# Kernel tuning notes

Measured on AMD Instinct MI355X. Metric: run time of the kernel, lower is better.

## Reference

```python
import jax, jax.numpy as jnp
import numpy as np

N = 50000      # number of genes
E = 1_600_000  # number of GRP edges
F = 256        # feature dim


def setup_inputs() -> dict:
    key = jax.random.key(0)
    k1, k2, k3 = jax.random.split(key, 3)
    indices = jax.random.randint(k1, (2, E), 0, N, dtype=jnp.int64 if jax.config.jax_enable_x64 else jnp.int32)
    values = jax.random.normal(k2, (E,), dtype=jnp.float32)
    mat_2 = jax.random.normal(k3, (N, F), dtype=jnp.float32)
    return {"indices": indices, "values": values, "n": N, "mat_2": mat_2}


def reference(indices, values, n, mat_2):
    # Sparse COO [n, n] @ dense [n, F]:
    # out[r] = sum over edges e with row[e]==r of values[e] * mat_2[col[e]]
    row, col = indices[0], indices[1]
    msgs = values[:, None] * mat_2[col]            # [E, F] gathered messages
    out = jax.ops.segment_sum(msgs, row, num_segments=n)  # [n, F]
    return out
```

## Files before the change

### kernel.cpp

```cpp
#include <hip/hip_runtime.h>

#define F_DIM   256
#define OVFCAP  8192
#define MAXBUCK 1024
#define BCAP    2560
#define P1_TILE 8192
#define WINB    13
#define MAXPASS 8
#define RCAP2   16
#define ELLK    64

struct OvfEdge { int r, c; float v; };

__device__ __forceinline__ unsigned short f32_to_bf16(float x) {
    unsigned u = __float_as_uint(x);
    unsigned r = (u + 0x7FFFu + ((u >> 16) & 1u)) >> 16;
    return (unsigned short)r;
}

__device__ __forceinline__ void gfma(unsigned e, int lane,
                                     const unsigned short* __restrict__ mb, float4& acc) {
    int   col = (int)(e >> 16);
    float v   = __uint_as_float((e & 0xFFFFu) << 16);
    ushort4 m = ((const ushort4*)(mb + ((long long)col << 8)))[lane];
    acc.x += v * __uint_as_float((unsigned)m.x << 16);
    acc.y += v * __uint_as_float((unsigned)m.y << 16);
    acc.z += v * __uint_as_float((unsigned)m.z << 16);
    acc.w += v * __uint_as_float((unsigned)m.w << 16);
}

__global__ void cvt_kernel(const float* __restrict__ src,
                           unsigned short* __restrict__ dst, int n4) {
    int t = blockIdx.x * blockDim.x + threadIdx.x;
    if (t >= n4) return;
    float4 f = ((const float4*)src)[t];
    ushort4 o;
    o.x = f32_to_bf16(f.x); o.y = f32_to_bf16(f.y);
    o.z = f32_to_bf16(f.z); o.w = f32_to_bf16(f.w);
    ((ushort4*)dst)[t] = o;
}

__global__ void __launch_bounds__(1024)
build_kernel(const int* __restrict__ rows, const int* __restrict__ cols,
             const float* __restrict__ vals,
             const float* __restrict__ mat2, unsigned short* __restrict__ mb, int n4,
             int* __restrict__ gcur, int2* __restrict__ ebuf,
             int* __restrict__ ovfcnt, OvfEdge* __restrict__ ovf,
             int E, int nbuck, int p1blocks) {
    __shared__ int s_cnt[MAXBUCK];
    __shared__ int s_base[MAXBUCK];
    __shared__ int s_cur[MAXBUCK];
    const int t = threadIdx.x;
    const int bid = blockIdx.x;

    if (bid >= p1blocks) {
        int i = (bid - p1blocks) * 1024 + t;
        if (i < n4) {
            float4 f = ((const float4*)mat2)[i];
            ushort4 o;
            o.x = f32_to_bf16(f.x); o.y = f32_to_bf16(f.y);
            o.z = f32_to_bf16(f.z); o.w = f32_to_bf16(f.w);
            ((ushort4*)mb)[i] = o;
        }
        return;
    }

    for (int i = t; i < nbuck; i += 1024) { s_cnt[i] = 0; s_cur[i] = 0; }
    __syncthreads();

    const long long e0 = (long long)bid * P1_TILE;
    int4 r4[2], c4[2]; float4 v4[2];
    #pragma unroll
    for (int k = 0; k < 2; ++k) {
        long long i = e0 + (long long)k * 4096 + (long long)t * 4;
        if (i + 3 < E) {
            r4[k] = *(const int4*)(rows + i);
            c4[k] = *(const int4*)(cols + i);
            v4[k] = *(const float4*)(vals + i);
        } else {
            r4[k] = make_int4(-1, -1, -1, -1);
            c4[k] = make_int4(0, 0, 0, 0);
            v4[k] = make_float4(0.f, 0.f, 0.f, 0.f);
            #pragma unroll
            for (int j = 0; j < 4; ++j) {
                long long ii = i + j;
                if (ii < E) {
                    (&r4[k].x)[j] = rows[ii];
                    (&c4[k].x)[j] = cols[ii];
                    (&v4[k].x)[j] = vals[ii];
                }
            }
        }
        #pragma unroll
        for (int j = 0; j < 4; ++j) {
            int rr = (&r4[k].x)[j];
            if (rr >= 0) atomicAdd(&s_cnt[rr >> 6], 1);
        }
    }
    __syncthreads();
    for (int i = t; i < nbuck; i += 1024) {
        int c_ = s_cnt[i];
        s_base[i] = c_ ? atomicAdd(&gcur[i], c_) : 0;
    }
    __syncthreads();
    #pragma unroll
    for (int k = 0; k < 2; ++k) {
        #pragma unroll
        for (int j = 0; j < 4; ++j) {
            int rr = (&r4[k].x)[j];
            if (rr < 0) continue;
            int cc = (&c4[k].x)[j];
            float vv = (&v4[k].x)[j];
            int b = rr >> 6;
            int sl = s_base[b] + atomicAdd(&s_cur[b], 1);
            if (sl < BCAP) {
                ebuf[(long long)b * BCAP + sl] =
                    make_int2((int)(((unsigned)cc << 16) | f32_to_bf16(vv)), rr & 63);
            } else {
                int o = atomicAdd(ovfcnt, 1);
                if (o < OVFCAP) { ovf[o].r = rr; ovf[o].c = cc; ovf[o].v = vv; }
            }
        }
    }
}

__global__ void __launch_bounds__(512, 6)
spmm_pass_kernel(const int* __restrict__ gcur, const int2* __restrict__ ebuf,
                 const unsigned short* __restrict__ mb,
                 float* __restrict__ out, int N,
                 int* __restrict__ ovfcnt, OvfEdge* __restrict__ ovf) {
    __shared__ int2 sorted[BCAP];
    __shared__ unsigned ell_s[2][64 * RCAP2];
    __shared__ int cur_s[2][64];
    __shared__ int pcnt[8][MAXPASS];
    __shared__ int pcur[8][MAXPASS];
    __shared__ int soff[64];

    const int t = threadIdx.x, b = blockIdx.x;
    const int wid = t >> 6, lane = t & 63;
    const int hw = t >> 5, fl = t & 31;
    const int npass = (N + (1 << WINB) - 1) >> WINB;
    const int cnt = min(gcur[b], BCAP);
    const int2* eb = ebuf + (long long)b * BCAP;

    if (t < 8 * MAXPASS) { ((int*)pcnt)[t] = 0; ((int*)pcur)[t] = 0; }
    if (t < 128) ((int*)cur_s)[t] = 0;
    #pragma unroll
    for (int q = 0; q < (2 * 64 * RCAP2) / 512; ++q) ((unsigned*)ell_s)[t + q * 512] = 0u;
    __syncthreads();

    int2 e4[5]; int pid[5]; int nv = 0;
    #pragma unroll
    for (int k = 0; k < 5; ++k) {
        int j = t + k * 512;
        if (j < cnt) {
            e4[nv] = eb[j];
            pid[nv] = (int)((unsigned)e4[nv].x >> (16 + WINB));
            atomicAdd(&pcnt[wid][pid[nv]], 1);
            ++nv;
        }
    }
    __syncthreads();

    if (wid == 0) {
        int val = pcnt[lane & 7][lane >> 3];
        int x = val;
        #pragma unroll
        for (int off = 1; off < 64; off <<= 1) {
            int y = __shfl_up(x, off);
            if (lane >= off) x += y;
        }
        soff[lane] = x - val;
    }
    __syncthreads();

    for (int k = 0; k < nv; ++k) {
        int p = pid[k];
        int pos = atomicAdd(&pcur[wid][p], 1);
        sorted[soff[p * 8 + wid] + pos] = e4[k];
    }
    __syncthreads();

    {
        int beg = soff[0];
        int end = (npass > 1) ? soff[8] : cnt;
        for (int j = beg + t; j < end; j += 512) {
            int2 e = sorted[j];
            int pos = atomicAdd(&cur_s[0][e.y], 1);
            if (pos < RCAP2) ell_s[0][(e.y << 4) | pos] = (unsigned)e.x;
            else {
                int o = atomicAdd(ovfcnt, 1);
                if (o < OVFCAP) {
                    ovf[o].r = b * 64 + e.y;
                    ovf[o].c = (int)((unsigned)e.x >> 16);
                    ovf[o].v = __uint_as_float(((unsigned)e.x & 0xFFFFu) << 16);
                }
            }
        }
    }
    __syncthreads();

    float acc[4][8];
    #pragma unroll
    for (int r = 0; r < 4; ++r)
        #pragma unroll
        for (int q = 0; q < 8; ++q) acc[r][q] = 0.f;

    for (int p = 0; p < npass; ++p) {
        const int cur = p & 1, nxt = cur ^ 1;

        if (p + 1 < npass) {
            int beg = soff[(p + 1) * 8];
            int end = (p + 2 < npass) ? soff[(p + 2) * 8] : cnt;
            for (int j = beg + t; j < end; j += 512) {
                int2 e = sorted[j];
                int pos = atomicAdd(&cur_s[nxt][e.y], 1);
                if (pos < RCAP2) ell_s[nxt][(e.y << 4) | pos] = (unsigned)e.x;
                else {
                    int o = atomicAdd(ovfcnt, 1);
                    if (o < OVFCAP) {
                        ovf[o].r = b * 64 + e.y;
                        ovf[o].c = (int)((unsigned)e.x >> 16);
                        ovf[o].v = __uint_as_float(((unsigned)e.x & 0xFFFFu) << 16);
                    }
                }
            }
        }

        #pragma unroll
        for (int ri = 0; ri < 4; ++ri) {
            const int rr = hw + (ri << 4);
            int deg = min(cur_s[cur][rr], RCAP2);
            int padded = (deg + 3) & ~3;
            for (int j = 0; j < padded; j += 4) {
                int4 m[4]; float v[4];
                #pragma unroll
                for (int k = 0; k < 4; ++k) {
                    unsigned e = ell_s[cur][(rr << 4) + j + k];
                    v[k] = __uint_as_float((e & 0xFFFFu) << 16);
                    m[k] = ((const int4*)(mb + ((long long)(e >> 16) << 8)))[fl];
                }
                #pragma unroll
                for (int k = 0; k < 4; ++k) {
                    acc[ri][0] += v[k] * __uint_as_float((unsigned)m[k].x << 16);
                    acc[ri][1] += v[k] * __uint_as_float((unsigned)m[k].x & 0xFFFF0000u);
                    acc[ri][2] += v[k] * __uint_as_float((unsigned)m[k].y << 16);
                    acc[ri][3] += v[k] * __uint_as_float((unsigned)m[k].y & 0xFFFF0000u);
                    acc[ri][4] += v[k] * __uint_as_float((unsigned)m[k].z << 16);
                    acc[ri][5] += v[k] * __uint_as_float((unsigned)m[k].z & 0xFFFF0000u);
                    acc[ri][6] += v[k] * __uint_as_float((unsigned)m[k].w << 16);
                    acc[ri][7] += v[k] * __uint_as_float((unsigned)m[k].w & 0xFFFF0000u);
                }
            }
            #pragma unroll
            for (int z = fl; z < RCAP2; z += 32) ell_s[cur][(rr << 4) + z] = 0u;
            if (fl == 0) cur_s[cur][rr] = 0;
        }
        __syncthreads();
    }

    #pragma unroll
    for (int ri = 0; ri < 4; ++ri) {
        const int rr = hw + (ri << 4);
        long long gr = (long long)b * 64 + rr;
        if (gr < N) {
            float4* op = (float4*)(out + (gr << 8) + (fl << 3));
            op[0] = make_float4(acc[ri][0], acc[ri][1], acc[ri][2], acc[ri][3]);
            op[1] = make_float4(acc[ri][4], acc[ri][5], acc[ri][6], acc[ri][7]);
        }
    }
}

__global__ void ovf_kernel(const int* __restrict__ ovfcnt,
                           const OvfEdge* __restrict__ ovf,
                           const float* __restrict__ mat2,
                           float* __restrict__ out) {
    int cnt = min(*ovfcnt, OVFCAP);
    int lane = threadIdx.x & 63;
    int wid = threadIdx.x >> 6;
    for (int e = wid; e < cnt; e += 4) {
        OvfEdge ed = ovf[e];
        float4 m = ((const float4*)(mat2 + (long long)ed.c * F_DIM))[lane];
        float* dst = out + (long long)ed.r * F_DIM + lane * 4;
        unsafeAtomicAdd(dst + 0, ed.v * m.x);
        unsafeAtomicAdd(dst + 1, ed.v * m.y);
        unsafeAtomicAdd(dst + 2, ed.v * m.z);
        unsafeAtomicAdd(dst + 3, ed.v * m.w);
    }
}

__device__ __forceinline__ void scatter_one(int r, int c, float v,
                                            int* cursor, unsigned* ell,
                                            int* ovfcnt, OvfEdge* ovf) {
    int pos = atomicAdd(&cursor[r], 1);
    if (pos < ELLK) {
        ell[(long long)r * ELLK + pos] = ((unsigned)c << 16) | f32_to_bf16(v);
    } else {
        int o = atomicAdd(ovfcnt, 1);
        if (o < OVFCAP) { ovf[o].r = r; ovf[o].c = c; ovf[o].v = v; }
    }
}

__global__ void scatter_ell_kernel(const int* __restrict__ rows,
                                   const int* __restrict__ cols,
                                   const float* __restrict__ vals,
                                   int* __restrict__ cursor,
                                   unsigned* __restrict__ ell,
                                   int* __restrict__ ovfcnt,
                                   OvfEdge* __restrict__ ovf, int E) {
    int t = blockIdx.x * blockDim.x + threadIdx.x;
    int i0 = t * 4;
    if (i0 + 3 < E) {
        int4   r = *(const int4*)(rows + i0);
        int4   c = *(const int4*)(cols + i0);
        float4 v = *(const float4*)(vals + i0);
        scatter_one(r.x, c.x, v.x, cursor, ell, ovfcnt, ovf);
        scatter_one(r.y, c.y, v.y, cursor, ell, ovfcnt, ovf);
        scatter_one(r.z, c.z, v.z, cursor, ell, ovfcnt, ovf);
        scatter_one(r.w, c.w, v.w, cursor, ell, ovfcnt, ovf);
    } else {
        for (int i = i0; i < E; ++i)
            scatter_one(rows[i], cols[i], vals[i], cursor, ell, ovfcnt, ovf);
    }
}

template <bool BF16MAT>
__global__ void __launch_bounds__(256)
spmm_ell_kernel(const int* __restrict__ cursor,
                const unsigned* __restrict__ ell,
                const unsigned short* __restrict__ mb,
                const float* __restrict__ mat2,
                float* __restrict__ out, int N) {
    int wave = (int)(((long long)blockIdx.x * blockDim.x + threadIdx.x) >> 6);
    int lane = threadIdx.x & 63;
    if (wave >= N) return;
    int deg = min(cursor[wave], ELLK);
    unsigned pk = (lane < deg) ? ell[(long long)wave * ELLK + lane] : 0u;
    float4 acc = make_float4(0.f, 0.f, 0.f, 0.f);
    int padded = (deg + 7) & ~7;
    for (int j = 0; j < padded; j += 8) {
        #pragma unroll
        for (int k = 0; k < 8; ++k) {
            unsigned e = (unsigned)__shfl((int)pk, j + k);
            if (BF16MAT) {
                gfma(e, lane, mb, acc);
            } else {
                int   col = (int)(e >> 16);
                float v   = __uint_as_float((e & 0xFFFFu) << 16);
                float4 m = ((const float4*)(mat2 + ((long long)col << 8)))[lane];
                acc.x += v * m.x; acc.y += v * m.y;
                acc.z += v * m.z; acc.w += v * m.w;
            }
        }
    }
    ((float4*)(out + ((long long)wave << 8)))[lane] = acc;
}

__global__ void spmm_atomic_kernel(const int* __restrict__ rows,
                                   const int* __restrict__ cols,
                                   const float* __restrict__ vals,
                                   const float* __restrict__ mat2,
                                   float* __restrict__ out, int E) {
    long long gid = (long long)blockIdx.x * blockDim.x + threadIdx.x;
    long long e = gid >> 6;
    int q = (int)(gid & 63);
    if (e >= E) return;
    int r = rows[e]; int c = cols[e]; float v = vals[e];
    float4 m = ((const float4*)(mat2 + (long long)c * F_DIM))[q];
    float* dst = out + (long long)r * F_DIM + q * 4;
    unsafeAtomicAdd(dst + 0, v * m.x);
    unsafeAtomicAdd(dst + 1, v * m.y);
    unsafeAtomicAdd(dst + 2, v * m.z);
    unsafeAtomicAdd(dst + 3, v * m.w);
}

extern "C" void kernel_launch(void* const* d_in, const int* in_sizes, int n_in,
                              void* d_out, int out_size, void* d_ws, size_t ws_size,
                              hipStream_t stream) {
    const int*   indices = (const int*)d_in[0];
    const float* vals    = (const float*)d_in[1];
    const float* mat2    = (const float*)d_in[3];
    float*       out     = (float*)d_out;

    const int E  = in_sizes[1];
    const int N  = out_size / F_DIM;
    const int M2 = in_sizes[3];
    const int n4 = M2 / 4;
    const int* rows = indices;
    const int* cols = indices + E;
    const int nbuck = (N + 63) >> 6;

    auto align16 = [](size_t x) { return (x + 15) & ~(size_t)15; };
    char* ws = (char*)d_ws;

    size_t o = 0;
    int* gcur    = (int*)(ws + o);
    int* ovfcntA = gcur + nbuck;
    o = align16(o + ((size_t)nbuck + 1) * 4);
    OvfEdge* ovfA = (OvfEdge*)(ws + o); o = align16(o + (size_t)OVFCAP * sizeof(OvfEdge));
    int2* ebuf = (int2*)(ws + o);       o = align16(o + (size_t)nbuck * BCAP * 8);
    unsigned short* mbA = (unsigned short*)(ws + o); o = align16(o + (size_t)M2 * 2);
    size_t need_A = o;

    o = 0;
    int* cursor  = (int*)(ws + o);
    int* ovfcntB = cursor + N;
    o = align16(o + ((size_t)N + 1) * 4);
    OvfEdge* ovfB = (OvfEdge*)(ws + o); o = align16(o + (size_t)OVFCAP * sizeof(OvfEdge));
    unsigned* ellB = (unsigned*)(ws + o); o = align16(o + (size_t)N * ELLK * 4);
    size_t need_mid = o;
    unsigned short* mbB = (unsigned short*)(ws + o); o = align16(o + (size_t)M2 * 2);
    size_t need_full = o;

    const int vblocks = ((E + 3) / 4 + 255) / 256;
    const int sblocks = (N * 64 + 255) / 256;
    const int cblocks = (n4 + 255) / 256;
    const int p1blocks = (E + P1_TILE - 1) / P1_TILE;

    if (N <= 65535 && nbuck <= MAXBUCK && ws_size >= need_A) {
        hipMemsetAsync(gcur, 0, ((size_t)nbuck + 1) * 4, stream);
        int bgrid = p1blocks + (n4 + 1023) / 1024;
        build_kernel<<<bgrid, 1024, 0, stream>>>(rows, cols, vals, mat2, mbA, n4,
                                                 gcur, ebuf, ovfcntA, ovfA, E, nbuck, p1blocks);
        spmm_pass_kernel<<<nbuck, 512, 0, stream>>>(gcur, ebuf, mbA, out, N, ovfcntA, ovfA);
        ovf_kernel<<<1, 256, 0, stream>>>(ovfcntA, ovfA, mat2, out);
    } else if (N <= 65535 && ws_size >= need_full) {
        hipMemsetAsync(cursor, 0, ((size_t)N + 1) * 4, stream);
        cvt_kernel<<<cblocks, 256, 0, stream>>>(mat2, mbB, n4);
        scatter_ell_kernel<<<vblocks, 256, 0, stream>>>(rows, cols, vals, cursor, ellB, ovfcntB, ovfB, E);
        spmm_ell_kernel<true><<<sblocks, 256, 0, stream>>>(cursor, ellB, mbB, mat2, out, N);
        ovf_kernel<<<1, 256, 0, stream>>>(ovfcntB, ovfB, mat2, out);
    } else if (N <= 65535 && ws_size >= need_mid) {
        hipMemsetAsync(cursor, 0, ((size_t)N + 1) * 4, stream);
        scatter_ell_kernel<<<vblocks, 256, 0, stream>>>(rows, cols, vals, cursor, ellB, ovfcntB, ovfB, E);
        spmm_ell_kernel<false><<<sblocks, 256, 0, stream>>>(cursor, ellB, mbB, mat2, out, N);
        ovf_kernel<<<1, 256, 0, stream>>>(ovfcntB, ovfB, mat2, out);
    } else {
        hipMemsetAsync(d_out, 0, (size_t)out_size * sizeof(float), stream);
        long long total = (long long)E * 64;
        spmm_atomic_kernel<<<(int)((total + 255) / 256), 256, 0, stream>>>(rows, cols, vals, mat2, out, E);
    }
}
```

Before: 175.9 us.

## Drop LDS counting sort in spmm pass kernel, bin edges from registers per pass

Removes the shared-memory sorted edge array and the per-wave pass counting sort. Each thread now keeps its edges in registers and rescans them every pass to bin them into the ELL buffers, with a narrower column window and smaller per-row capacity. Padding slots are masked to a valid in-window dummy entry rather than cleared, and the inner unroll drops from 4 to 2. The smaller LDS footprint allows a higher occupancy target (launch bounds 8), at the cost of rescanning all edges each pass, running twice as many passes, and sending more edges to the global overflow path.

Result: slower. 196.6 us (+11.7%).

```diff
diff --git a/kernel.cpp b/kernel.cpp
--- a/kernel.cpp
+++ b/kernel.cpp
@@ -5,9 +5,8 @@
 #define MAXBUCK 1024
 #define BCAP    2560
 #define P1_TILE 8192
-#define WINB    13
-#define MAXPASS 8
-#define RCAP2   16
+#define WINB    12
+#define RCAP2   12
 #define ELLK    64
 
 struct OvfEdge { int r, c; float v; };
@@ -124,80 +123,53 @@
     }
 }
 
-__global__ void __launch_bounds__(512, 6)
+__global__ void __launch_bounds__(512, 8)
 spmm_pass_kernel(const int* __restrict__ gcur, const int2* __restrict__ ebuf,
                  const unsigned short* __restrict__ mb,
                  float* __restrict__ out, int N,
                  int* __restrict__ ovfcnt, OvfEdge* __restrict__ ovf) {
-    __shared__ int2 sorted[BCAP];
     __shared__ unsigned ell_s[2][64 * RCAP2];
     __shared__ int cur_s[2][64];
-    __shared__ int pcnt[8][MAXPASS];
-    __shared__ int pcur[8][MAXPASS];
-    __shared__ int soff[64];
-
     const int t = threadIdx.x, b = blockIdx.x;
-    const int wid = t >> 6, lane = t & 63;
     const int hw = t >> 5, fl = t & 31;
     const int npass = (N + (1 << WINB) - 1) >> WINB;
     const int cnt = min(gcur[b], BCAP);
     const int2* eb = ebuf + (long long)b * BCAP;
 
-    if (t < 8 * MAXPASS) { ((int*)pcnt)[t] = 0; ((int*)pcur)[t] = 0; }
     if (t < 128) ((int*)cur_s)[t] = 0;
-    #pragma unroll
-    for (int q = 0; q < (2 * 64 * RCAP2) / 512; ++q) ((unsigned*)ell_s)[t + q * 512] = 0u;
-    __syncthreads();
-
-    int2 e4[5]; int pid[5]; int nv = 0;
+
+    unsigned ecol[5]; int erow[5]; int nv = 0;
     #pragma unroll
     for (int k = 0; k < 5; ++k) {
         int j = t + k * 512;
         if (j < cnt) {
-            e4[nv] = eb[j];
-            pid[nv] = (int)((unsigned)e4[nv].x >> (16 + WINB));
-            atomicAdd(&pcnt[wid][pid[nv]], 1);
+            int2 e = eb[j];
+            ecol[nv] = (unsigned)e.x;
+            erow[nv] = e.y;
             ++nv;
         }
     }
     __syncthreads();
 
-    if (wid == 0) {
-        int val = pcnt[lane & 7][lane >> 3];
-        int x = val;
-        #pragma unroll
-        for (int off = 1; off < 64; off <<= 1) {
-            int y = __shfl_up(x, off);
-            if (lane >= off) x += y;
-        }
-        soff[lane] = x - val;
-    }
-    __syncthreads();
-
-    for (int k = 0; k < nv; ++k) {
-        int p = pid[k];
-        int pos = atomicAdd(&pcur[wid][p], 1);
-        sorted[soff[p * 8 + wid] + pos] = e4[k];
-    }
-    __syncthreads();
-
-    {
-        int beg = soff[0];
-        int end = (npass > 1) ? soff[8] : cnt;
-        for (int j = beg + t; j < end; j += 512) {
-            int2 e = sorted[j];
-            int pos = atomicAdd(&cur_s[0][e.y], 1);
-            if (pos < RCAP2) ell_s[0][(e.y << 4) | pos] = (unsigned)e.x;
-            else {
-                int o = atomicAdd(ovfcnt, 1);
-                if (o < OVFCAP) {
-                    ovf[o].r = b * 64 + e.y;
-                    ovf[o].c = (int)((unsigned)e.x >> 16);
-                    ovf[o].v = __uint_as_float(((unsigned)e.x & 0xFFFFu) << 16);
+    auto bin = [&](int p, int buf) {
+        for (int k = 0; k < nv; ++k) {
+            if ((int)(ecol[k] >> (16 + WINB)) == p) {
+                int pos = atomicAdd(&cur_s[buf][erow[k]], 1);
+                if (pos < RCAP2) {
+                    ell_s[buf][erow[k] * RCAP2 + pos] = ecol[k];
+                } else {
+                    int o = atomicAdd(ovfcnt, 1);
+                    if (o < OVFCAP) {
+                        ovf[o].r = b * 64 + erow[k];
+                        ovf[o].c = (int)(ecol[k] >> 16);
+                        ovf[o].v = __uint_as_float((ecol[k] & 0xFFFFu) << 16);
+                    }
                 }
             }
         }
-    }
+    };
+
+    bin(0, 0);
     __syncthreads();
 
     float acc[4][8];
@@ -208,40 +180,25 @@
 
     for (int p = 0; p < npass; ++p) {
         const int cur = p & 1, nxt = cur ^ 1;
-
-        if (p + 1 < npass) {
-            int beg = soff[(p + 1) * 8];
-            int end = (p + 2 < npass) ? soff[(p + 2) * 8] : cnt;
-            for (int j = beg + t; j < end; j += 512) {
-                int2 e = sorted[j];
-                int pos = atomicAdd(&cur_s[nxt][e.y], 1);
-                if (pos < RCAP2) ell_s[nxt][(e.y << 4) | pos] = (unsigned)e.x;
-                else {
-                    int o = atomicAdd(ovfcnt, 1);
-                    if (o < OVFCAP) {
-                        ovf[o].r = b * 64 + e.y;
-                        ovf[o].c = (int)((unsigned)e.x >> 16);
-                        ovf[o].v = __uint_as_float(((unsigned)e.x & 0xFFFFu) << 16);
-                    }
-                }
-            }
-        }
-
+        if (p + 1 < npass) bin(p + 1, nxt);
+
+        const unsigned padv = (unsigned)p << (16 + WINB);
         #pragma unroll
         for (int ri = 0; ri < 4; ++ri) {
             const int rr = hw + (ri << 4);
             int deg = min(cur_s[cur][rr], RCAP2);
-            int padded = (deg + 3) & ~3;
-            for (int j = 0; j < padded; j += 4) {
-                int4 m[4]; float v[4];
+            int padded = (deg + 1) & ~1;
+            for (int j = 0; j < padded; j += 2) {
+                int4 m[2]; float v[2];
                 #pragma unroll
-                for (int k = 0; k < 4; ++k) {
-                    unsigned e = ell_s[cur][(rr << 4) + j + k];
+                for (int k = 0; k < 2; ++k) {
+                    unsigned raw = ell_s[cur][rr * RCAP2 + j + k];
+                    unsigned e = (j + k < deg) ? raw : padv;
                     v[k] = __uint_as_float((e & 0xFFFFu) << 16);
                     m[k] = ((const int4*)(mb + ((long long)(e >> 16) << 8)))[fl];
                 }
                 #pragma unroll
-                for (int k = 0; k < 4; ++k) {
+                for (int k = 0; k < 2; ++k) {
                     acc[ri][0] += v[k] * __uint_as_float((unsigned)m[k].x << 16);
                     acc[ri][1] += v[k] * __uint_as_float((unsigned)m[k].x & 0xFFFF0000u);
                     acc[ri][2] += v[k] * __uint_as_float((unsigned)m[k].y << 16);
@@ -252,8 +209,6 @@
                     acc[ri][7] += v[k] * __uint_as_float((unsigned)m[k].w & 0xFFFF0000u);
                 }
             }
-            #pragma unroll
-            for (int z = fl; z < RCAP2; z += 32) ell_s[cur][(rr << 4) + z] = 0u;
             if (fl == 0) cur_s[cur][rr] = 0;
         }
         __syncthreads();
```
